# Kernel tuning notes

Measured on AMD Instinct MI355X. Metric: run time of the kernel, lower is better.

## Reference

```python
import jax, jax.numpy as jnp
import numpy as np

N = 10000      # nodes
D_IN = 12      # exact in-degree per node (regular graph -> static triplet count)
E = N * D_IN   # 120000 directed edges
T = E * D_IN   # 1440000 triplets (k->i for each edge i->j)
K_R = 16
K_A = 8
HID = 64
OUT = 32
R_GAMMA = 8.0  # 1/(2*((4.0-0.0)/16)**2)
A_GAMMA = 8.0  # 1/(2*(2.0/8)**2)
EPS = 1e-8


def setup_inputs() -> dict:
    rng = np.random.default_rng(0)
    # edge e: row[e] -> col[e]; edges sorted by destination so in-edges of node i are [i*D_IN,(i+1)*D_IN)
    col = np.repeat(np.arange(N, dtype=np.int64), D_IN)
    row = rng.integers(0, N, size=E, dtype=np.int64)
    # triplets: for each edge e (i=row[e], j=col[e]), all D_IN edges k->i
    e_e = np.repeat(np.arange(E, dtype=np.int64), D_IN)                      # [T]
    ki_idx = (row[:, None] * D_IN + np.arange(D_IN)[None, :]).reshape(-1)    # [T] indices of k->i edges
    k_e = row[ki_idx]
    i_e = row[e_e]
    j_e = col[e_e]

    key = jax.random.key(0)
    kp, k1, k2 = jax.random.split(key, 3)
    pos = jax.random.normal(kp, (N, 3), dtype=jnp.float32) * 2.0
    in_dim = 2 * K_R + K_A
    W1 = jax.random.normal(k1, (in_dim, HID), dtype=jnp.float32) / np.sqrt(in_dim)
    b1 = jnp.zeros((HID,), dtype=jnp.float32)
    W2 = jax.random.normal(k2, (HID, OUT), dtype=jnp.float32) / np.sqrt(HID)
    b2 = jnp.zeros((OUT,), dtype=jnp.float32)
    r_centers = jnp.linspace(0.0, 4.0, K_R, dtype=jnp.float32)
    a_centers = jnp.linspace(-1.0, 1.0, K_A, dtype=jnp.float32)
    return {
        "pos": pos, "W1": W1, "b1": b1, "W2": W2, "b2": b2,
        "r_centers": r_centers, "a_centers": a_centers,
        "e_e": jnp.asarray(e_e, dtype=jnp.int32),
        "i_e": jnp.asarray(i_e, dtype=jnp.int32),
        "j_e": jnp.asarray(j_e, dtype=jnp.int32),
        "k_e": jnp.asarray(k_e, dtype=jnp.int32),
    }


def _rbf(x, centers, gamma):
    # x: [T,1], centers: [K] -> [T,K]
    return jnp.exp(-gamma * (x - centers[None, :]) ** 2)


def reference(pos, W1, b1, W2, b2, r_centers, a_centers, e_e, i_e, j_e, k_e):
    rij = pos[j_e] - pos[i_e]                 # [T,3]
    rik = pos[k_e] - pos[i_e]                 # [T,3]
    dij = jnp.linalg.norm(rij, axis=-1, keepdims=True)
    dik = jnp.linalg.norm(rik, axis=-1, keepdims=True)
    cos_theta = jnp.clip(jnp.sum(rij * rik, axis=-1, keepdims=True) / (dij * dik + EPS), -1.0, 1.0)
    feat = jnp.concatenate(
        [_rbf(dij, r_centers, R_GAMMA), _rbf(dik, r_centers, R_GAMMA), _rbf(cos_theta, a_centers, A_GAMMA)],
        axis=-1,
    )                                          # [T, 2*K_R+K_A]
    h = jax.nn.silu(feat @ W1 + b1)            # [T, HID]
    emb = h @ W2 + b2                          # [T, OUT]
    # exclude k == j triplets (torch masks them out before scatter)
    emb = emb * (k_e != j_e)[:, None].astype(emb.dtype)
    return jax.ops.segment_sum(emb, e_e, num_segments=E)  # [E, OUT]
```

## Files before the change

kernel.cpp:

```cpp
#include <hip/hip_runtime.h>
#include <hip/hip_bf16.h>
#include <math.h>

#define N_GROUPS 7500
#define HID 64
#define OUTC 32
#define EPSV 1e-8f
#define C2G  (-11.54156032f)
#define LOG2E 1.44269504f
#define CSR  (4.0f / 15.0f)
#define CSA  (2.0f / 7.0f)

typedef __bf16 bf16x8 __attribute__((ext_vector_type(8)));
typedef float  f32x4  __attribute__((ext_vector_type(4)));
typedef unsigned short u16x4 __attribute__((ext_vector_type(4)));

#define WAVES 4
#define BLOCK 256
#define GRID 1875

__global__ __launch_bounds__(BLOCK, 4) void gemnet_mfma_kernel(
    const float* __restrict__ pos,
    const float* __restrict__ W1, const float* __restrict__ b1,
    const float* __restrict__ W2, const float* __restrict__ b2,
    const int* __restrict__ i_e, const int* __restrict__ k_e,
    float* __restrict__ out)
{
    __shared__ __align__(16) unsigned short hbuf[WAVES][2][16 * HID];

    const int tid  = threadIdx.x;
    const int w    = tid >> 6;
    const int lane = tid & 63;
    const int tl16 = lane & 15;
    const int g    = lane >> 4;
    const int sw   = (tl16 & 7) << 3;

    bf16x8 a1d[4];
#pragma unroll
    for (int mt = 0; mt < 4; ++mt) {
#pragma unroll
        for (int e = 0; e < 8; ++e) {
            float v = 0.0f;
            if (e < 4)       v = W1[(16 + 4 * g + e) * HID + mt * 16 + tl16];
            else if (e == 4) v = W1[(32 + 2 * g) * HID + mt * 16 + tl16];
            else if (e == 5) v = W1[(32 + 2 * g + 1) * HID + mt * 16 + tl16];
            a1d[mt][e] = (__bf16)v;
        }
    }
    bf16x8 au[4];
#pragma unroll
    for (int mt = 0; mt < 4; ++mt) {
#pragma unroll
        for (int e = 0; e < 8; ++e) {
            float v = 0.0f;
            if (e < 4)                 v = W1[(4 * g + e) * HID + mt * 16 + tl16];
            else if (e == 4 && g == 0) v = b1[mt * 16 + tl16];
            au[mt][e] = (__bf16)v;
        }
    }
    bf16x8 a2[2][2];
#pragma unroll
    for (int mt = 0; mt < 2; ++mt)
#pragma unroll
        for (int ks = 0; ks < 2; ++ks)
#pragma unroll
            for (int e = 0; e < 8; ++e)
                a2[mt][ks][e] = (__bf16)W2[(ks * 32 + g * 8 + e) * OUTC + mt * 16 + tl16];
    f32x4 b2v0, b2v1;
#pragma unroll
    for (int r = 0; r < 4; ++r) { b2v0[r] = b2[4 * g + r]; b2v1[r] = b2[16 + 4 * g + r]; }

    const f32x4 fz = {0.f, 0.f, 0.f, 0.f};
    const float gofs_r4 = (float)(4 * g) * CSR;
    const float gofs_a  = (float)(2 * g) * CSA - 1.0f;

    const int grp    = blockIdx.x * WAVES + w;
    const int e_lane = grp * 16 + tl16;
    const int tlane  = e_lane * 12;
    const int j      = e_lane / 12;

    const int4 kq0 = *(const int4*)&k_e[tlane];
    const int4 kq1 = *(const int4*)&k_e[tlane + 4];
    const int4 kq2 = *(const int4*)&k_e[tlane + 8];
    const int kv[12] = {kq0.x, kq0.y, kq0.z, kq0.w,
                        kq1.x, kq1.y, kq1.z, kq1.w,
                        kq2.x, kq2.y, kq2.z, kq2.w};

    const int   i   = i_e[tlane];
    const float pix = pos[3 * i], piy = pos[3 * i + 1], piz = pos[3 * i + 2];
    const float rijx = pos[3 * j] - pix, rijy = pos[3 * j + 1] - piy, rijz = pos[3 * j + 2] - piz;
    const float dij = __builtin_amdgcn_sqrtf(rijx * rijx + rijy * rijy + rijz * rijz);

    float Pkx[12], Pky[12], Pkz[12];
#pragma unroll
    for (int m = 0; m < 12; ++m) {
        const int k = kv[m];
        Pkx[m] = pos[3 * k];
        Pky[m] = pos[3 * k + 1];
        Pkz[m] = pos[3 * k + 2];
    }

    bf16x8 bu;
    {
        const float dco = dij - gofs_r4;
#pragma unroll
        for (int e = 0; e < 8; ++e) {
            float v = 0.0f;
            if (e < 4) {
                const float x = dco - (float)e * CSR;
                v = __builtin_amdgcn_exp2f(C2G * x * x);
            } else if (e == 4 && g == 0) v = 1.0f;
            bu[e] = (__bf16)v;
        }
    }
    f32x4 accu[4];
#pragma unroll
    for (int mt = 0; mt < 4; ++mt)
        accu[mt] = __builtin_amdgcn_mfma_f32_16x16x32_bf16(au[mt], bu, fz, 0, 0, 0);

    f32x4 D0 = fz, D1 = fz;
    float cntf = 0.0f;

#pragma unroll
    for (int m = 0; m < 12; ++m) {
        const float rikx = Pkx[m] - pix, riky = Pky[m] - piy, rikz = Pkz[m] - piz;
        const float dik = __builtin_amdgcn_sqrtf(rikx * rikx + riky * riky + rikz * rikz);
        const float dotv = rijx * rikx + rijy * riky + rijz * rikz;
        float cosv = dotv * __builtin_amdgcn_rcpf(dij * dik + EPSV);
        cosv = fminf(1.0f, fmaxf(-1.0f, cosv));

        const float dco = dik - gofs_r4;
        const float Aq  = C2G * dco * dco;
        const float Bn  = (-2.0f * C2G * CSR) * dco;
        bf16x8 bm;
#pragma unroll
        for (int e = 0; e < 4; ++e) {
            const float arg = fmaf((float)e, Bn, Aq) + (C2G * CSR * CSR) * (float)(e * e);
            bm[e] = (__bf16)__builtin_amdgcn_exp2f(arg);
        }
        const float cco = cosv - gofs_a;
        bm[4] = (__bf16)__builtin_amdgcn_exp2f(C2G * cco * cco);
        const float cc1 = cco - CSA;
        bm[5] = (__bf16)__builtin_amdgcn_exp2f(C2G * cc1 * cc1);
        bm[6] = (__bf16)0.0f;
        bm[7] = (__bf16)0.0f;

        f32x4 acc1[4];
#pragma unroll
        for (int mt = 0; mt < 4; ++mt)
            acc1[mt] = __builtin_amdgcn_mfma_f32_16x16x32_bf16(a1d[mt], bm, accu[mt], 0, 0, 0);

        const u16x4 hz = {0, 0, 0, 0};
        const bool keep = (kv[m] != j);
        cntf += keep ? 1.0f : 0.0f;
#pragma unroll
        for (int mt = 0; mt < 4; ++mt) {
            u16x4 hw;
#pragma unroll
            for (int r = 0; r < 4; ++r) {
                const float v = acc1[mt][r];
                const float sv = v * __builtin_amdgcn_rcpf(1.0f + __builtin_amdgcn_exp2f(-LOG2E * v));
                hw[r] = __builtin_bit_cast(unsigned short, (__bf16)sv);
            }
            hw = keep ? hw : hz;
            const int colW = (mt * 16 + 4 * g) ^ sw;
            *(u16x4*)&hbuf[w][m & 1][tl16 * HID + colW] = hw;
        }
        const bf16x8 hb0 = *(const bf16x8*)&hbuf[w][m & 1][tl16 * HID + ((8 * g) ^ sw)];
        const bf16x8 hb1 = *(const bf16x8*)&hbuf[w][m & 1][tl16 * HID + ((32 + 8 * g) ^ sw)];

        D0 = __builtin_amdgcn_mfma_f32_16x16x32_bf16(a2[0][0], hb0, D0, 0, 0, 0);
        D0 = __builtin_amdgcn_mfma_f32_16x16x32_bf16(a2[0][1], hb1, D0, 0, 0, 0);
        D1 = __builtin_amdgcn_mfma_f32_16x16x32_bf16(a2[1][0], hb0, D1, 0, 0, 0);
        D1 = __builtin_amdgcn_mfma_f32_16x16x32_bf16(a2[1][1], hb1, D1, 0, 0, 0);
    }

#pragma unroll
    for (int r = 0; r < 4; ++r) {
        D0[r] = fmaf(cntf, b2v0[r], D0[r]);
        D1[r] = fmaf(cntf, b2v1[r], D1[r]);
    }

    const int rbase = e_lane * OUTC;
    *(f32x4*)&out[rbase + 4 * g]      = D0;
    *(f32x4*)&out[rbase + 16 + 4 * g] = D1;
}

extern "C" void kernel_launch(void* const* d_in, const int* in_sizes, int n_in,
                              void* d_out, int out_size, void* d_ws, size_t ws_size,
                              hipStream_t stream) {
    const float* pos = (const float*)d_in[0];
    const float* W1  = (const float*)d_in[1];
    const float* b1  = (const float*)d_in[2];
    const float* W2  = (const float*)d_in[3];
    const float* b2  = (const float*)d_in[4];
    const int* i_e = (const int*)d_in[8];
    const int* k_e = (const int*)d_in[10];
    float* out = (float*)d_out;

    gemnet_mfma_kernel<<<GRID, BLOCK, 0, stream>>>(
        pos, W1, b1, W2, b2, i_e, k_e, out);
}
```

Baseline: 47.59 us.

## Software-pipeline k-position loads and defer second GEMM by one iteration

Measured after the change: 46.44 us. 1.02x faster.

```diff
diff --git a/kernel.cpp b/kernel.cpp
--- a/kernel.cpp
+++ b/kernel.cpp
@@ -91,15 +91,6 @@
     const float rijx = pos[3 * j] - pix, rijy = pos[3 * j + 1] - piy, rijz = pos[3 * j + 2] - piz;
     const float dij = __builtin_amdgcn_sqrtf(rijx * rijx + rijy * rijy + rijz * rijz);
 
-    float Pkx[12], Pky[12], Pkz[12];
-#pragma unroll
-    for (int m = 0; m < 12; ++m) {
-        const int k = kv[m];
-        Pkx[m] = pos[3 * k];
-        Pky[m] = pos[3 * k + 1];
-        Pkz[m] = pos[3 * k + 2];
-    }
-
     bf16x8 bu;
     {
         const float dco = dij - gofs_r4;
@@ -121,9 +112,18 @@
     f32x4 D0 = fz, D1 = fz;
     float cntf = 0.0f;
 
+    float ckx = pos[3 * kv[0]], cky = pos[3 * kv[0] + 1], ckz = pos[3 * kv[0] + 2];
+    bf16x8 hb0p, hb1p;
+
 #pragma unroll
     for (int m = 0; m < 12; ++m) {
-        const float rikx = Pkx[m] - pix, riky = Pky[m] - piy, rikz = Pkz[m] - piz;
+        float nkx = 0.f, nky = 0.f, nkz = 0.f;
+        if (m < 11) {
+            const int kn = kv[m + 1];
+            nkx = pos[3 * kn]; nky = pos[3 * kn + 1]; nkz = pos[3 * kn + 2];
+        }
+
+        const float rikx = ckx - pix, riky = cky - piy, rikz = ckz - piz;
         const float dik = __builtin_amdgcn_sqrtf(rikx * rikx + riky * riky + rikz * rikz);
         const float dotv = rijx * rikx + rijy * riky + rijz * rikz;
         float cosv = dotv * __builtin_amdgcn_rcpf(dij * dik + EPSV);
@@ -149,6 +149,13 @@
 #pragma unroll
         for (int mt = 0; mt < 4; ++mt)
             acc1[mt] = __builtin_amdgcn_mfma_f32_16x16x32_bf16(a1d[mt], bm, accu[mt], 0, 0, 0);
+
+        if (m > 0) {
+            D0 = __builtin_amdgcn_mfma_f32_16x16x32_bf16(a2[0][0], hb0p, D0, 0, 0, 0);
+            D0 = __builtin_amdgcn_mfma_f32_16x16x32_bf16(a2[0][1], hb1p, D0, 0, 0, 0);
+            D1 = __builtin_amdgcn_mfma_f32_16x16x32_bf16(a2[1][0], hb0p, D1, 0, 0, 0);
+            D1 = __builtin_amdgcn_mfma_f32_16x16x32_bf16(a2[1][1], hb1p, D1, 0, 0, 0);
+        }
 
         const u16x4 hz = {0, 0, 0, 0};
         const bool keep = (kv[m] != j);
@@ -166,14 +173,16 @@
             const int colW = (mt * 16 + 4 * g) ^ sw;
             *(u16x4*)&hbuf[w][m & 1][tl16 * HID + colW] = hw;
         }
-        const bf16x8 hb0 = *(const bf16x8*)&hbuf[w][m & 1][tl16 * HID + ((8 * g) ^ sw)];
-        const bf16x8 hb1 = *(const bf16x8*)&hbuf[w][m & 1][tl16 * HID + ((32 + 8 * g) ^ sw)];
-
-        D0 = __builtin_amdgcn_mfma_f32_16x16x32_bf16(a2[0][0], hb0, D0, 0, 0, 0);
-        D0 = __builtin_amdgcn_mfma_f32_16x16x32_bf16(a2[0][1], hb1, D0, 0, 0, 0);
-        D1 = __builtin_amdgcn_mfma_f32_16x16x32_bf16(a2[1][0], hb0, D1, 0, 0, 0);
-        D1 = __builtin_amdgcn_mfma_f32_16x16x32_bf16(a2[1][1], hb1, D1, 0, 0, 0);
-    }
+        hb0p = *(const bf16x8*)&hbuf[w][m & 1][tl16 * HID + ((8 * g) ^ sw)];
+        hb1p = *(const bf16x8*)&hbuf[w][m & 1][tl16 * HID + ((32 + 8 * g) ^ sw)];
+
+        ckx = nkx; cky = nky; ckz = nkz;
+    }
+
+    D0 = __builtin_amdgcn_mfma_f32_16x16x32_bf16(a2[0][0], hb0p, D0, 0, 0, 0);
+    D0 = __builtin_amdgcn_mfma_f32_16x16x32_bf16(a2[0][1], hb1p, D0, 0, 0, 0);
+    D1 = __builtin_amdgcn_mfma_f32_16x16x32_bf16(a2[1][0], hb0p, D1, 0, 0, 0);
+    D1 = __builtin_amdgcn_mfma_f32_16x16x32_bf16(a2[1][1], hb1p, D1, 0, 0, 0);
 
 #pragma unroll
     for (int r = 0; r < 4; ++r) {
```
